# Kernel tuning notes

Measured on AMD Instinct MI355X. Metric: run time of the kernel, lower is better.

Reference implementation:

```python
import jax, jax.numpy as jnp
from jax import lax
import numpy as np

B, T, F = 4, 16000, 512          # batch, frames, enc_num_feats
NB = 24                          # 3 stacks x 8 layers
DILS = [2 ** l for _ in range(3) for l in range(8)]


def _prelu(x, a):
    return jnp.where(x >= 0, x, a * x)


def _conv(x, w, stride=1, pad=0, dil=1, groups=1):
    # x: [B,C,T], w: [O, C//groups, K]
    return lax.conv_general_dilated(x, w, (stride,), [(pad, pad)], rhs_dilation=(dil,),
                                    dimension_numbers=('NCH', 'OIH', 'NCH'),
                                    feature_group_count=groups)


def _tconv(x, w, stride=1):
    # torch ConvTranspose1d, weight layout [in, out, k], padding=0
    k = w.shape[-1]
    wf = jnp.flip(w, -1).transpose(1, 0, 2)  # [out, in, k]
    return lax.conv_general_dilated(x, wf, (1,), [(k - 1, k - 1)], lhs_dilation=(stride,),
                                    dimension_numbers=('NCH', 'OIH', 'NCH'))


def _pw(x, w, b):
    # 1x1 conv as GEMM; w: [O,C], b: [O]
    return jnp.einsum('oc,bct->bot', w, x) + b[:, None]


def _branch(x, p):
    # encoder
    f = _conv(x, p['enc_w0'], stride=8)                       # [B,512,1999]
    f = _prelu(_conv(f, p['enc_w1']), p['enc_a'][0])          # [B,512,1997]
    f = _prelu(_conv(f, p['enc_w2']), p['enc_a'][1])          # [B,512,1995]
    # mask generator (TCN)
    o = _pw(f, p['mg_in_w'], p['mg_in_b'])                    # [B,128,t]
    for i in range(NB):
        d = DILS[i]
        h = _prelu(_pw(o, p['blk_w1'][i], p['blk_b1'][i]), p['blk_a1'][i])     # [B,32,t]
        h = _conv(h, p['blk_dw'][i][:, None, :], pad=d, dil=d, groups=32) + p['blk_db'][i][:, None]
        h = _prelu(h, p['blk_a2'][i])
        if i < NB - 1:  # last block has no residual path
            o = o + _pw(h, p['blk_rw'][i], p['blk_rb'][i])
        o = o + _pw(h, p['blk_sw'][i], p['blk_sb'][i])
    m = jax.nn.sigmoid(_pw(_prelu(o, p['mg_out_a']), p['mg_out_w'], p['mg_out_b']))  # [B,1024,t]
    b, _, t = f.shape
    m = m.reshape(b, 2, F, t)
    y = (m * f[:, None]).reshape(b * 2, F, t)
    # decoder
    y = _prelu(_tconv(y, p['dec_w1']), p['dec_a'][0])
    y = _prelu(_tconv(y, p['dec_w2']), p['dec_a'][1])
    y = _tconv(y, p['dec_w3'], stride=8)                      # [2B,1,T]
    return y.reshape(b, 2, -1)


_NAMES = ['x_real', 'x_imag', 'enc_w0', 'enc_w1', 'enc_w2', 'enc_a', 'mg_in_w', 'mg_in_b',
          'blk_w1', 'blk_b1', 'blk_a1', 'blk_dw', 'blk_db', 'blk_a2', 'blk_rw', 'blk_rb',
          'blk_sw', 'blk_sb', 'mg_out_a', 'mg_out_w', 'mg_out_b', 'dec_w1', 'dec_w2', 'dec_a', 'dec_w3']


def _forward(*args):
    p = dict(zip(_NAMES, args))
    out_r = _branch(p['x_real'], p)
    out_i = _branch(p['x_imag'], p)
    return jnp.stack([out_r, out_i])  # [2, B, 2, T]; axis0 = (real, imag)


def setup_inputs() -> dict:
    key = jax.random.key(0)
    ks = jax.random.split(key, 16)
    n = lambda k, s, sc: jax.random.normal(k, s, dtype=jnp.float32) * sc
    f32 = jnp.float32
    return {
        'x_real': jax.random.normal(ks[0], (B, 1, T), dtype=f32),
        'x_imag': jax.random.normal(ks[1], (B, 1, T), dtype=f32),
        'enc_w0': n(ks[2], (512, 1, 16), 0.1),
        'enc_w1': n(ks[3], (512, 512, 3), 0.03),
        'enc_w2': n(ks[4], (512, 512, 3), 0.03),
        'enc_a': jnp.full((2,), 0.25, f32),
        'mg_in_w': n(ks[5], (128, 512), 0.05),
        'mg_in_b': jnp.zeros((128,), f32),
        'blk_w1': n(ks[6], (NB, 32, 128), 0.08),
        'blk_b1': jnp.zeros((NB, 32), f32),
        'blk_a1': jnp.full((NB,), 0.25, f32),
        'blk_dw': n(ks[7], (NB, 32, 3), 0.2),
        'blk_db': jnp.zeros((NB, 32), f32),
        'blk_a2': jnp.full((NB,), 0.25, f32),
        'blk_rw': n(ks[8], (NB, 128, 32), 0.08),  # index NB-1 unused (no_residual)
        'blk_rb': jnp.zeros((NB, 128), f32),
        'blk_sw': n(ks[9], (NB, 128, 32), 0.08),
        'blk_sb': jnp.zeros((NB, 128), f32),
        'mg_out_a': jnp.asarray(0.25, f32),
        'mg_out_w': n(ks[10], (1024, 128), 0.08),
        'mg_out_b': jnp.zeros((1024,), f32),
        'dec_w1': n(ks[11], (512, 512, 3), 0.03),
        'dec_w2': n(ks[12], (512, 512, 3), 0.03),
        'dec_a': jnp.full((2,), 0.25, f32),
        'dec_w3': n(ks[13], (512, 1, 16), 0.1),
    }


def reference(x_real, x_imag, enc_w0, enc_w1, enc_w2, enc_a, mg_in_w, mg_in_b,
              blk_w1, blk_b1, blk_a1, blk_dw, blk_db, blk_a2, blk_rw, blk_rb,
              blk_sw, blk_sb, mg_out_a, mg_out_w, mg_out_b, dec_w1, dec_w2, dec_a, dec_w3):
    return _forward(x_real, x_imag, enc_w0, enc_w1, enc_w2, enc_a, mg_in_w, mg_in_b,
                    blk_w1, blk_b1, blk_a1, blk_dw, blk_db, blk_a2, blk_rw, blk_rb,
                    blk_sw, blk_sb, mg_out_a, mg_out_w, mg_out_b, dec_w1, dec_w2, dec_a, dec_w3)
```

## Files before the change

kernel.cpp:

```cpp
#include <hip/hip_runtime.h>
#include <hip/hip_cooperative_groups.h>

namespace cg = cooperative_groups;


typedef unsigned short u16;
typedef __attribute__((ext_vector_type(8))) short bf16x8_t;
typedef __attribute__((ext_vector_type(4))) float f32x4_t;

#define ST    2064
#define HALO  8
#define TR    2064
#define RHALO 8

#define U_F0H   0ULL
#define U_F1H   8454144ULL
#define F_F2    8454144ULL
#define F_D2    0ULL
#define U_YH    33816576ULL
#define U_D1H   50724864ULL
#define F_O     33816576ULL
#define F_G0    35930112ULL
#define F_G1    36458496ULL
#define F_W     36986880ULL
#define W_MGIN  0ULL
#define W_MGOUT 65536ULL
#define W_W1T   196608ULL
#define W_WSUMT 294912ULL
#define W_BSUM  393216ULL
#define U_WB    74766336ULL
#define F_FLAG  38956032ULL
#define F_G2    38964224ULL
#define F_G3    39492608ULL
#define U_MGB   73973760ULL
#define U_MKB   74104832ULL
#define U_W1B   74375168ULL
#define U_WSB   74563584ULL

#define WS_HI 0
#define WS_LO 5120
#define W1_HI 10240
#define W1_LO 14592
#define OB_HI 0
#define OB_LO 8704
#define HB_HI 0
#define HB_LO 2560

__device__ __forceinline__ float prelu_f(float x, float a) { return x >= 0.f ? x : a * x; }
__device__ __forceinline__ u16 f2b(float f) {
    unsigned u = __float_as_uint(f);
    return (u16)((u + 0x7FFF + ((u >> 16) & 1)) >> 16);
}
__device__ __forceinline__ float b2f(u16 h) {
    return __uint_as_float((unsigned)h << 16);
}
__device__ __forceinline__ void gload16(const void* g, void* l) {
    __builtin_amdgcn_global_load_lds(
        (const __attribute__((address_space(1))) unsigned*)g,
        (__attribute__((address_space(3))) unsigned*)l, 16, 0, 0);
}

__global__ __launch_bounds__(256) void prep_all(
    const float* __restrict__ ew1, const float* __restrict__ ew2,
    const float* __restrict__ dw1, const float* __restrict__ dw2,
    const float* __restrict__ mgin_w, const float* __restrict__ mgout_w,
    const float* __restrict__ bw1, const float* __restrict__ brw,
    const float* __restrict__ brb, const float* __restrict__ bsw,
    const float* __restrict__ bsb, float* __restrict__ wsf, u16* __restrict__ wsb,
    unsigned* __restrict__ flags)
{
    const int task = blockIdx.y;
    const int idx  = blockIdx.x * 256 + threadIdx.x;
    const int stride = gridDim.x * 256;
    if (task < 4) {
        const float* src = (task == 0) ? ew1 : (task == 1) ? ew2 : (task == 2) ? dw1 : dw2;
        u16* dst = wsb + U_WB + (size_t)task * 786432ULL;
        const bool dec = (task >= 2);
        for (int n = idx; n < 786432; n += stride) {
            int j = n >> 18, o = (n >> 9) & 511, c = n & 511;
            float v = dec ? src[(size_t)c * 1536 + o * 3 + (2 - j)]
                          : src[(size_t)o * 1536 + c * 3 + j];
            dst[n] = f2b(v);
        }
    } else if (task == 4) {
        u16* dst = wsb + U_MGB;
        for (int n = idx; n < 131072; n += stride) {
            int C = n & 511, m = (n >> 9) & 127, p = n >> 16;
            float v = mgin_w[(size_t)m * 512 + C];
            u16 hh = f2b(v);
            if (p) hh = f2b(v - b2f(hh));
            dst[n] = hh;
        }
    } else if (task == 5) {
        u16* dst = wsb + U_MKB;
        for (int n = idx; n < 262144; n += stride) {
            int C = n & 127, m = (n >> 7) & 1023, p = n >> 17;
            float v = mgout_w[(size_t)m * 128 + C];
            u16 hh = f2b(v);
            if (p) hh = f2b(v - b2f(hh));
            dst[n] = hh;
        }
    } else if (task == 6) {
        float* dstf = wsf + F_W + W_W1T;
        for (int n = idx; n < 4096; n += stride) {
            int cc = n & 31, C = n >> 5;
            dstf[n] = bw1[(size_t)cc * 128 + C];
        }
        u16* dstb = wsb + U_W1B;
        for (int n = idx; n < 188416; n += stride) {
            int C = n & 127, cgi = (n >> 7) & 31, p = (n >> 12) & 1, ii = n >> 13;
            float v = bw1[(size_t)(ii + 1) * 4096 + cgi * 128 + C];
            u16 hh = f2b(v);
            if (p) hh = f2b(v - b2f(hh));
            dstb[n] = hh;
        }
    } else if (task == 7) {
        u16* dst = wsb + U_WSB;
        for (int n = idx; n < 196608; n += stride) {
            int cc = n & 31, C = (n >> 5) & 127, p = (n >> 12) & 1, i = n >> 13;
            float v = bsw[(size_t)i * 4096 + C * 32 + cc];
            if (i < 23) v += brw[(size_t)i * 4096 + C * 32 + cc];
            u16 hh = f2b(v);
            if (p) hh = f2b(v - b2f(hh));
            dst[n] = hh;
        }
    } else if (task == 8) {
        float* dst = wsf + F_W + W_BSUM;
        for (int n = idx; n < 3072; n += stride) {
            int i = n >> 7;
            float v = bsb[n];
            if (i < 23) v += brb[n];
            dst[n] = v;
        }
    } else if (task == 9) {
        const unsigned long long uoff[4] = { U_F0H, U_F1H, U_YH, U_D1H };
        const int nbArr[4]   = { 8, 8, 16, 16 };
        const int trArr[4]   = { 1999, 1997, 1995, 1997 };
#pragma unroll
        for (int z = 0; z < 4; z++) {
            unsigned* base = (unsigned*)(wsb + uoff[z]);
            const int nb = nbArr[z], Treal = trArr[z];
            const int prcnt = TR - Treal;
            const int total = nb * prcnt * 256;
            for (int n = idx; n < total; n += stride) {
                const int col = n & 255;
                const int r   = n >> 8;
                const int bb  = r / prcnt;
                const int pr  = r % prcnt;
                const int row = (pr < RHALO) ? pr : (Treal + pr);
                base[((size_t)bb * TR + row) * 256 + col] = 0u;
            }
        }
    } else {
        for (int n = idx; n < 4096; n += stride) flags[n] = 0u;
    }
}

__global__ __launch_bounds__(256) void enc0_kernel(
    const float* __restrict__ xr, const float* __restrict__ xi,
    const float* __restrict__ w0, u16* __restrict__ f0h)
{
    const int t  = blockIdx.x * 256 + threadIdx.x;
    const int c0 = blockIdx.y * 8;
    const int b  = blockIdx.z;
    if (t >= 1999) return;
    const float* x = (b < 4) ? (xr + (size_t)b * 16000) : (xi + (size_t)(b - 4) * 16000);
    float xv[16];
    const int base = t * 8;
#pragma unroll
    for (int k = 0; k < 16; k++) xv[k] = x[base + k];
    union { u16 u[8]; uint4 v; } p;
#pragma unroll
    for (int cq = 0; cq < 8; cq++) {
        const float* w = w0 + (size_t)(c0 + cq) * 16;
        float acc = 0.f;
#pragma unroll
        for (int k = 0; k < 16; k++) acc = fmaf(xv[k], w[k], acc);
        p.u[cq] = f2b(acc);
    }
    *(uint4*)&f0h[((size_t)b * TR + RHALO + t) * 512 + c0] = p.v;
}

template <int JOFF, int OUTF32, int TT>
__global__ __launch_bounds__(256) void conv_mfma(
    const u16* __restrict__ in, u16* __restrict__ out16, float* __restrict__ out32,
    const u16* __restrict__ wM, const float* __restrict__ alpha_p, int Tout)
{
    constexpr int NF    = TT / 32;
    constexpr int BFULL = TT / 64;
    constexpr int SMEMSZ = (TT == 128) ? 17408 : 14464;
    __shared__ __align__(16) u16 smem[SMEMSZ];
    u16* As = smem;
    u16* Bs = smem + 12288;
    const int tid  = threadIdx.x;
    const int t0   = blockIdx.x * TT;
    const int ob   = blockIdx.y * 128;
    const int b    = blockIdx.z;
    const int l15  = tid & 15;
    const int quad = (tid >> 4) & 3;
    const int wave = tid >> 6;
    const int wm   = (wave & 1) * 64;
    const int wn   = (wave >> 1) * (TT / 2);
    const u16* inb = in + (size_t)b * TR * 512;
    const int wvb  = wave * 1024;

    f32x4_t acc[4][NF];
#pragma unroll
    for (int i = 0; i < 4; i++)
#pragma unroll
        for (int k = 0; k < NF; k++) acc[i][k] = (f32x4_t){0.f, 0.f, 0.f, 0.f};

    for (int c0 = 0; c0 < 512; c0 += 32) {
#pragma unroll
        for (int k = 0; k < 6; k++) {
            const int v = k * 256 + tid;
            const int j = v >> 9, r = (v >> 2) & 127, c = v & 3;
            const int cg = c ^ ((r >> 1) & 3);
            gload16(&wM[((size_t)(j * 512 + ob + r)) * 512 + c0 + cg * 8],
                    (char*)As + k * 4096 + wvb);
        }
#pragma unroll
        for (int k = 0; k < BFULL; k++) {
            const int v = k * 256 + tid;
            const int r = v >> 2, c = v & 3;
            const int cg = c ^ ((r >> 1) & 3);
            gload16(&inb[(size_t)(RHALO + t0 + JOFF + r) * 512 + c0 + cg * 8],
                    (char*)Bs + k * 4096 + wvb);
        }
        if (tid < 16) {
            const int v = BFULL * 256 + tid;
            const int r = v >> 2, c = v & 3;
            const int cg = c ^ ((r >> 1) & 3);
            gload16(&inb[(size_t)(RHALO + t0 + JOFF + r) * 512 + c0 + cg * 8],
                    (char*)Bs + BFULL * 4096);
        }
        __syncthreads();
#pragma unroll
        for (int j = 0; j < 3; j++) {
            bf16x8_t aw[4], bi[NF];
#pragma unroll
            for (int mf = 0; mf < 4; mf++) {
                const int row = wm + mf * 16 + l15;
                const int ch  = quad ^ ((row >> 1) & 3);
                aw[mf] = *(const bf16x8_t*)&As[j * 4096 + row * 32 + ch * 8];
            }
#pragma unroll
            for (int nf = 0; nf < NF; nf++) {
                const int row = wn + nf * 16 + l15 + j;
                const int ch  = quad ^ ((row >> 1) & 3);
                bi[nf] = *(const bf16x8_t*)&Bs[row * 32 + ch * 8];
            }
#pragma unroll
            for (int mf = 0; mf < 4; mf++)
#pragma unroll
                for (int nf = 0; nf < NF; nf++) {
                    if (OUTF32)
                        acc[mf][nf] = __builtin_amdgcn_mfma_f32_16x16x32_bf16(
                            bi[nf], aw[mf], acc[mf][nf], 0, 0, 0);
                    else
                        acc[mf][nf] = __builtin_amdgcn_mfma_f32_16x16x32_bf16(
                            aw[mf], bi[nf], acc[mf][nf], 0, 0, 0);
                }
        }
        __syncthreads();
    }

    const float alpha = *alpha_p;
    if (!OUTF32) {
        u16* tile = smem;
#pragma unroll
        for (int mf = 0; mf < 4; mf++)
#pragma unroll
            for (int nf = 0; nf < NF; nf++) {
                const int t_loc = wn + nf * 16 + l15;
                const int c_loc = wm + mf * 16 + quad * 4;
                f32x4_t a = acc[mf][nf];
                ushort4 s;
                s.x = f2b(prelu_f(a.x, alpha));
                s.y = f2b(prelu_f(a.y, alpha));
                s.z = f2b(prelu_f(a.z, alpha));
                s.w = f2b(prelu_f(a.w, alpha));
                *(ushort4*)&tile[t_loc * 136 + c_loc] = s;
            }
        __syncthreads();
        for (int v = tid; v < TT * 16; v += 256) {
            const int row = v >> 4, seg = v & 15;
            const int t = t0 + row;
            if (t < Tout)
                *(uint4*)&out16[((size_t)b * TR + RHALO + t) * 512 + ob + seg * 8] =
                    *(const uint4*)&tile[row * 136 + seg * 8];
        }
    } else {
#pragma unroll
        for (int mf = 0; mf < 4; mf++)
#pragma unroll
            for (int nf = 0; nf < NF; nf++) {
                const int o  = ob + wm + mf * 16 + l15;
                const int tb = t0 + wn + nf * 16 + quad * 4;
                f32x4_t a = acc[mf][nf];
                float v0 = prelu_f(a.x, alpha), v1 = prelu_f(a.y, alpha);
                float v2 = prelu_f(a.z, alpha), v3 = prelu_f(a.w, alpha);
                float* p = out32 + ((size_t)(b * 512 + o)) * ST + HALO + tb;
                if (tb + 3 < Tout) {
                    *(float4*)p = make_float4(v0, v1, v2, v3);
                } else {
                    if (tb + 0 < Tout) p[0] = v0;
                    if (tb + 1 < Tout) p[1] = v1;
                    if (tb + 2 < Tout) p[2] = v2;
                    if (tb + 3 < Tout) p[3] = v3;
                }
            }
    }
}

__global__ __launch_bounds__(256) void mgin_kernel(
    const float* __restrict__ f2, float* __restrict__ o_buf, float* __restrict__ g_out,
    const u16* __restrict__ wA, const float* __restrict__ bias,
    const float* __restrict__ w1T0, const float* __restrict__ b1_0,
    const float* __restrict__ a1_0)
{
    __shared__ __align__(16) u16   As[8192];
    __shared__ __align__(16) u16   Bsm[5120];
    __shared__ __align__(16) float o_lds[128 * 68];
    const int tid = threadIdx.x;
    const int t0  = blockIdx.x * 64;
    const int b   = blockIdx.y;
    const int l15 = tid & 15, quad = (tid >> 4) & 3, wave = tid >> 6;
    const int wm  = wave * 32;
    const int bc  = tid >> 3;
    const int bs  = tid & 7;

    f32x4_t acc[2][4];
#pragma unroll
    for (int mf = 0; mf < 2; mf++)
#pragma unroll
        for (int nf = 0; nf < 4; nf++) acc[mf][nf] = (f32x4_t){0.f, 0.f, 0.f, 0.f};

    for (int ks = 0; ks < 16; ks++) {
#pragma unroll
        for (int k = 0; k < 4; k++) {
            const int v = k * 256 + tid;
            const int p = v >> 9, r = (v >> 2) & 127, c = v & 3;
            const int cg = c ^ ((r >> 1) & 3);
            gload16(&wA[(size_t)p * 65536 + (size_t)r * 512 + ks * 32 + cg * 8],
                    (char*)As + k * 4096 + wave * 1024);
        }
        {
            const float* src = f2 + (size_t)(b * 512 + ks * 32 + bc) * ST + HALO + t0 + bs * 8;
            float4 v0 = *(const float4*)src;
            float4 v1 = *(const float4*)(src + 4);
            const float vv[8] = {v0.x, v0.y, v0.z, v0.w, v1.x, v1.y, v1.z, v1.w};
#pragma unroll
            for (int j = 0; j < 8; j++) {
                const int t = bs * 8 + j;
                const u16 hh = f2b(vv[j]);
                Bsm[t * 40 + bc] = hh;
                Bsm[2560 + t * 40 + bc] = f2b(vv[j] - b2f(hh));
            }
        }
        __syncthreads();
        bf16x8_t ah[2], al[2], bh[4], bl[4];
#pragma unroll
        for (int mf = 0; mf < 2; mf++) {
            const int row = wm + mf * 16 + l15;
            const int ch  = quad ^ ((row >> 1) & 3);
            ah[mf] = *(const bf16x8_t*)&As[row * 32 + ch * 8];
            al[mf] = *(const bf16x8_t*)&As[4096 + row * 32 + ch * 8];
        }
#pragma unroll
        for (int nf = 0; nf < 4; nf++) {
            const int rt = nf * 16 + l15;
            bh[nf] = *(const bf16x8_t*)&Bsm[rt * 40 + quad * 8];
            bl[nf] = *(const bf16x8_t*)&Bsm[2560 + rt * 40 + quad * 8];
        }
#pragma unroll
        for (int mf = 0; mf < 2; mf++)
#pragma unroll
            for (int nf = 0; nf < 4; nf++) {
                acc[mf][nf] = __builtin_amdgcn_mfma_f32_16x16x32_bf16(al[mf], bh[nf], acc[mf][nf], 0, 0, 0);
                acc[mf][nf] = __builtin_amdgcn_mfma_f32_16x16x32_bf16(ah[mf], bl[nf], acc[mf][nf], 0, 0, 0);
                acc[mf][nf] = __builtin_amdgcn_mfma_f32_16x16x32_bf16(ah[mf], bh[nf], acc[mf][nf], 0, 0, 0);
            }
        __syncthreads();
    }

#pragma unroll
    for (int mf = 0; mf < 2; mf++)
#pragma unroll
        for (int nf = 0; nf < 4; nf++) {
#pragma unroll
            for (int r = 0; r < 4; r++) {
                const int m = wm + mf * 16 + quad * 4 + r;
                o_lds[m * 68 + nf * 16 + l15] = acc[mf][nf][r] + bias[m];
            }
        }
    __syncthreads();

    for (int n = tid; n < 2048; n += 256) {
        const int row = n >> 4, seg = n & 15;
        const int tb = t0 + seg * 4;
        float* dst = o_buf + (size_t)(b * 128 + row) * ST + HALO + tb;
        const float* srcl = &o_lds[row * 68 + seg * 4];
        if (tb + 3 < 1995) {
            *(float4*)dst = *(const float4*)srcl;
        } else {
#pragma unroll
            for (int kk = 0; kk < 4; kk++)
                if (tb + kk < 1995) dst[kk] = srcl[kk];
        }
    }

    const int t = tid & 63, cg_ = tid >> 6;
    const float a1 = *a1_0;
    float acc2[8];
#pragma unroll
    for (int q = 0; q < 8; q++) acc2[q] = b1_0[cg_ * 8 + q];
    for (int C = 0; C < 128; C++) {
        const float ov = o_lds[C * 68 + t];
        const float4* wr = (const float4*)(w1T0 + (size_t)C * 32 + cg_ * 8);
        float4 w0 = wr[0], w1 = wr[1];
        acc2[0] = fmaf(w0.x, ov, acc2[0]); acc2[1] = fmaf(w0.y, ov, acc2[1]);
        acc2[2] = fmaf(w0.z, ov, acc2[2]); acc2[3] = fmaf(w0.w, ov, acc2[3]);
        acc2[4] = fmaf(w1.x, ov, acc2[4]); acc2[5] = fmaf(w1.y, ov, acc2[5]);
        acc2[6] = fmaf(w1.z, ov, acc2[6]); acc2[7] = fmaf(w1.w, ov, acc2[7]);
    }
    const int tt = t0 + t;
    if (tt < 1995) {
#pragma unroll
        for (int q = 0; q < 8; q++)
            g_out[(size_t)(b * 32 + cg_ * 8 + q) * ST + HALO + tt] = prelu_f(acc2[q], a1);
    }
}

__device__ __forceinline__ void poll_acquire(const unsigned* flags, int b, int j,
                                             int k, unsigned target)
{
    int lo = j - k; if (lo < 0) lo = 0;
    int hi = j + k; if (hi > 31) hi = 31;
    for (int n = lo; n <= hi; n++) {
        if (n == j) continue;
        const unsigned* p = flags + ((b << 5) + n) * 16;
        while (__hip_atomic_load(p, __ATOMIC_RELAXED, __HIP_MEMORY_SCOPE_AGENT) < target)
            __builtin_amdgcn_s_sleep(2);
    }
    __builtin_amdgcn_fence(__ATOMIC_ACQUIRE, "agent");
}

__device__ __forceinline__ void store_pair_agent(float* dst, int trel, float v0, float v1)
{
    if (trel + 1 < 1995) {
        unsigned long long raw =
            ((unsigned long long)__float_as_uint(v1) << 32) | __float_as_uint(v0);
        __hip_atomic_store((unsigned long long*)dst, raw,
                           __ATOMIC_RELAXED, __HIP_MEMORY_SCOPE_AGENT);
    } else if (trel < 1995) {
        __hip_atomic_store(dst, v0, __ATOMIC_RELAXED, __HIP_MEMORY_SCOPE_AGENT);
    }
}

__global__ __launch_bounds__(512) void tcn_fused(
    float* __restrict__ g0, float* __restrict__ g1,
    float* __restrict__ g2, float* __restrict__ g3,
    float* __restrict__ o_buf,
    const float* __restrict__ dw_all, const float* __restrict__ db_all,
    const float* __restrict__ a2_all,
    const u16* __restrict__ wsb16, const float* __restrict__ bsum_all,
    const u16* __restrict__ w1b16, const float* __restrict__ b1_all,
    const float* __restrict__ a1_all, unsigned* __restrict__ wflag)
{
    __shared__ __align__(16) u16  wbuf[18944];
    __shared__ __align__(16) u16  hbuf[5120];
    __shared__ __align__(16) u16  ob16[17408];
    __shared__ __align__(16) float g_lds[2][2176];
    __shared__ __align__(16) float halo_lds[8320];

    const int tid = threadIdx.x;
    const int blk = blockIdx.x;
    const int b   = blk & 7;
    const int jt  = blk >> 3;
    const int t0  = jt * 64;
    float* gbuf[4] = { g0, g1, g2, g3 };

    const int wv   = tid >> 6;
    const int l15  = tid & 15;
    const int quad = (tid >> 4) & 3;
    const int Cb   = wv * 16 + quad * 4;

    f32x4_t o_acc[4];
#pragma unroll
    for (int k = 0; k < 4; k++)
#pragma unroll
        for (int r = 0; r < 4; r++)
            o_acc[k][r] = o_buf[((size_t)(b * 128 + Cb + r)) * ST + HALO + t0 + k * 16 + l15];
    {
        int cc = tid >> 4, seg = tid & 15;
        *(float4*)&g_lds[0][cc * 68 + seg * 4] =
            *(const float4*)&g0[((size_t)(b * 32 + cc)) * ST + HALO + t0 + seg * 4];
    }

    for (int i = 0; i < 24; i++) {
        const int dil  = 1 << (i & 7);
        const int dil2 = (dil < 2) ? 2 : dil;
        const int k_rd = (dil > 64) ? 2 : 1;
        const float* gin_g = gbuf[i & 3];
        float* gout_g      = gbuf[(i + 1) & 3];
        float* gin_lds  = g_lds[i & 1];
        float* gout_lds = g_lds[(i + 1) & 1];

        {
            const u16* wsg = wsb16 + (size_t)i * 8192;
#pragma unroll
            for (int k = 0; k < 2; k++) {
                int c = tid + k * 512;
                int p = c >> 9, r = (c >> 2) & 127, s = c & 3;
                *(uint4*)&wbuf[(p ? WS_LO : WS_HI) + r * 40 + s * 8] =
                    *(const uint4*)&wsg[c * 8];
            }
            if (i < 23) {
                const u16* w1g = w1b16 + (size_t)i * 8192;
#pragma unroll
                for (int k = 0; k < 2; k++) {
                    int c = tid + k * 512;
                    int p = c >> 9, cgi = (c >> 4) & 31, s = c & 15;
                    *(uint4*)&wbuf[(p ? W1_LO : W1_HI) + cgi * 136 + s * 8] =
                        *(const uint4*)&w1g[c * 8];
                }
            }
        }

        if (i > 0 && tid == 0) poll_acquire(wflag, b, jt, k_rd, (unsigned)i);
        __syncthreads();

        {
            const int dsh = (dil2 >= 128) ? 7 : (dil2 >= 64) ? 6 : (dil2 >= 32) ? 5
                          : (dil2 >= 16) ? 4 : (dil2 >= 8) ? 3 : (dil2 >= 4) ? 2 : 1;
            const int total = 32 << dsh;
            for (int n = tid; n < total; n += 512) {
                const int cc = n >> dsh;
                const int pi = n & (dil2 - 1);
                const int hc = pi * 2;
                const int tg = (hc < dil2) ? (t0 - dil2 + hc) : (t0 + 64 + hc - dil2);
                float v0 = 0.f, v1 = 0.f;
                const float* src = gin_g + ((size_t)(b * 32 + cc)) * ST + HALO + tg;
                if (tg >= 0 && tg + 1 < 1995) {
                    unsigned long long raw = __hip_atomic_load(
                        (const unsigned long long*)src,
                        __ATOMIC_RELAXED, __HIP_MEMORY_SCOPE_AGENT);
                    v0 = __uint_as_float((unsigned)raw);
                    v1 = __uint_as_float((unsigned)(raw >> 32));
                } else {
                    if (tg >= 0 && tg < 1995)
                        v0 = __hip_atomic_load(src, __ATOMIC_RELAXED,
                                               __HIP_MEMORY_SCOPE_AGENT);
                    if (tg + 1 >= 0 && tg + 1 < 1995)
                        v1 = __hip_atomic_load(src + 1, __ATOMIC_RELAXED,
                                               __HIP_MEMORY_SCOPE_AGENT);
                }
                halo_lds[cc * 260 + hc]     = v0;
                halo_lds[cc * 260 + hc + 1] = v1;
            }
        }
        __syncthreads();

        {
            const float a2 = a2_all[i];
            const int t = tid & 63, cc0 = (tid >> 6) * 4;
            const int tt = t0 + t;
            ushort4 hi4, lo4;
            u16 hs[4], ls[4];
#pragma unroll
            for (int q = 0; q < 4; q++) {
                const int cc = cc0 + q;
                const float w0 = dw_all[i * 96 + cc * 3 + 0];
                const float w1v = dw_all[i * 96 + cc * 3 + 1];
                const float w2 = dw_all[i * 96 + cc * 3 + 2];
                const float ctr = gin_lds[cc * 68 + t];
                float lo = 0.f, hi = 0.f;
                const int tm = tt - dil;
                if (tm >= 0)
                    lo = (tm >= t0) ? gin_lds[cc * 68 + (tm - t0)]
                                    : halo_lds[cc * 260 + (tm - t0 + dil2)];
                const int tp = tt + dil;
                if (tp < 1995)
                    hi = (tp < t0 + 64) ? gin_lds[cc * 68 + (tp - t0)]
                                        : halo_lds[cc * 260 + (dil2 + tp - t0 - 64)];
                float s = db_all[i * 32 + cc] + w1v * ctr;
                s = fmaf(w0, lo, s);
                s = fmaf(w2, hi, s);
                const float hval = prelu_f(s, a2);
                const u16 hh = f2b(hval);
                hs[q] = hh;
                ls[q] = f2b(hval - b2f(hh));
            }
            hi4.x = hs[0]; hi4.y = hs[1]; hi4.z = hs[2]; hi4.w = hs[3];
            lo4.x = ls[0]; lo4.y = ls[1]; lo4.z = ls[2]; lo4.w = ls[3];
            *(ushort4*)&hbuf[HB_HI + t * 40 + cc0] = hi4;
            *(ushort4*)&hbuf[HB_LO + t * 40 + cc0] = lo4;
        }
        __syncthreads();

        {
            const bf16x8_t a_hi = *(const bf16x8_t*)&wbuf[WS_HI + (wv * 16 + l15) * 40 + quad * 8];
            const bf16x8_t a_lo = *(const bf16x8_t*)&wbuf[WS_LO + (wv * 16 + l15) * 40 + quad * 8];
            const float4 bs4 = *(const float4*)&bsum_all[i * 128 + Cb];
#pragma unroll
            for (int k = 0; k < 4; k++) {
                const bf16x8_t b_hi = *(const bf16x8_t*)&hbuf[HB_HI + (k * 16 + l15) * 40 + quad * 8];
                const bf16x8_t b_lo = *(const bf16x8_t*)&hbuf[HB_LO + (k * 16 + l15) * 40 + quad * 8];
                f32x4_t acc = o_acc[k];
                acc = __builtin_amdgcn_mfma_f32_16x16x32_bf16(a_lo, b_hi, acc, 0, 0, 0);
                acc = __builtin_amdgcn_mfma_f32_16x16x32_bf16(a_hi, b_lo, acc, 0, 0, 0);
                acc = __builtin_amdgcn_mfma_f32_16x16x32_bf16(a_hi, b_hi, acc, 0, 0, 0);
                acc.x += bs4.x; acc.y += bs4.y; acc.z += bs4.z; acc.w += bs4.w;
                o_acc[k] = acc;
            }
        }

        if (i == 23) break;

#pragma unroll
        for (int k = 0; k < 4; k++) {
            ushort4 hi4, lo4;
            u16 hs[4], ls[4];
#pragma unroll
            for (int r = 0; r < 4; r++) {
                const float v = o_acc[k][r];
                const u16 hh = f2b(v);
                hs[r] = hh;
                ls[r] = f2b(v - b2f(hh));
            }
            hi4.x = hs[0]; hi4.y = hs[1]; hi4.z = hs[2]; hi4.w = hs[3];
            lo4.x = ls[0]; lo4.y = ls[1]; lo4.z = ls[2]; lo4.w = ls[3];
            const int t_loc = k * 16 + l15;
            *(ushort4*)&ob16[OB_HI + t_loc * 136 + Cb] = hi4;
            *(ushort4*)&ob16[OB_LO + t_loc * 136 + Cb] = lo4;
        }
        __syncthreads();

        {
            const int cgb = (wv & 1) * 16;
            const int tb  = (wv >> 1) * 16;
            const float4 b14 = *(const float4*)&b1_all[(i + 1) * 32 + cgb + quad * 4];
            f32x4_t ga = (f32x4_t){b14.x, b14.y, b14.z, b14.w};
            f32x4_t gc = (f32x4_t){0.f, 0.f, 0.f, 0.f};
#pragma unroll
            for (int slab = 0; slab < 4; slab++) {
                const bf16x8_t wa_hi = *(const bf16x8_t*)&wbuf[W1_HI + (cgb + l15) * 136 + slab * 32 + quad * 8];
                const bf16x8_t wa_lo = *(const bf16x8_t*)&wbuf[W1_LO + (cgb + l15) * 136 + slab * 32 + quad * 8];
                const bf16x8_t obh   = *(const bf16x8_t*)&ob16[OB_HI + (tb + l15) * 136 + slab * 32 + quad * 8];
                const bf16x8_t obl   = *(const bf16x8_t*)&ob16[OB_LO + (tb + l15) * 136 + slab * 32 + quad * 8];
                if (slab & 1) {
                    gc = __builtin_amdgcn_mfma_f32_16x16x32_bf16(wa_lo, obh, gc, 0, 0, 0);
                    gc = __builtin_amdgcn_mfma_f32_16x16x32_bf16(wa_hi, obl, gc, 0, 0, 0);
                    gc = __builtin_amdgcn_mfma_f32_16x16x32_bf16(wa_hi, obh, gc, 0, 0, 0);
                } else {
                    ga = __builtin_amdgcn_mfma_f32_16x16x32_bf16(wa_lo, obh, ga, 0, 0, 0);
                    ga = __builtin_amdgcn_mfma_f32_16x16x32_bf16(wa_hi, obl, ga, 0, 0, 0);
                    ga = __builtin_amdgcn_mfma_f32_16x16x32_bf16(wa_hi, obh, ga, 0, 0, 0);
                }
            }
            const float a1 = a1_all[i + 1];
#pragma unroll
            for (int r = 0; r < 4; r++) {
                const int cgr = cgb + quad * 4 + r;
                gout_lds[cgr * 68 + tb + l15] = prelu_f(ga[r] + gc[r], a1);
            }
        }
        __syncthreads();

        {
            const int dnext = 1 << ((i + 1) & 7);
            int md2 = (dnext > 64) ? 64 : dnext;
            if (md2 < 2) md2 = 2;
            if (md2 >= 64) {
                for (int n = tid; n < 1024; n += 512) {
                    const int cc = n >> 5, pi = n & 31;
                    const int lt = pi * 2;
                    float* dst = gout_g + ((size_t)(b * 32 + cc)) * ST + HALO + t0 + lt;
                    store_pair_agent(dst, t0 + lt,
                                     gout_lds[cc * 68 + lt], gout_lds[cc * 68 + lt + 1]);
                }
            } else {
                const int msh = (md2 >= 32) ? 5 : (md2 >= 16) ? 4 : (md2 >= 8) ? 3
                              : (md2 >= 4) ? 2 : 1;
                const int total = 32 << msh;
                for (int n = tid; n < total; n += 512) {
                    const int cc = n >> msh;
                    const int pi = n & (md2 - 1);
                    const int hc = pi * 2;
                    const int lt = (hc < md2) ? hc : (64 - 2 * md2 + hc);
                    float* dst = gout_g + ((size_t)(b * 32 + cc)) * ST + HALO + t0 + lt;
                    store_pair_agent(dst, t0 + lt,
                                     gout_lds[cc * 68 + lt], gout_lds[cc * 68 + lt + 1]);
                }
            }
        }
        __syncthreads();

        if (tid == 0)
            __hip_atomic_store(&wflag[((b << 5) + jt) * 16], (unsigned)(i + 1),
                               __ATOMIC_RELAXED, __HIP_MEMORY_SCOPE_AGENT);
    }

#pragma unroll
    for (int k = 0; k < 4; k++)
#pragma unroll
        for (int r = 0; r < 4; r++)
            o_buf[((size_t)(b * 128 + Cb + r)) * ST + HALO + t0 + k * 16 + l15] = o_acc[k][r];
}

__global__ __launch_bounds__(256) void mask_kernel(
    const float* __restrict__ o_buf, const float* __restrict__ f2, u16* __restrict__ yh,
    const u16* __restrict__ wA, const float* __restrict__ mb,
    const float* __restrict__ a_out_p)
{
    __shared__ __align__(16) u16 smem[33792];
    u16* As = smem;
    u16* ob = smem + 16384;

    const int tid  = threadIdx.x;
    const int t0   = blockIdx.x * 64;
    const int m0   = blockIdx.y * 256;
    const int b    = blockIdx.z;
    const float ao = *a_out_p;
    const int l15  = tid & 15;
    const int quad = (tid >> 4) & 3;
    const int wave = tid >> 6;
    const int wm   = wave * 64;

    {
        const int C = tid >> 1, th = (tid & 1) * 32;
        const float* orow = o_buf + (size_t)(b * 128 + C) * ST + HALO + t0 + th;
#pragma unroll
        for (int q = 0; q < 8; q++) {
            float4 v = *(const float4*)(orow + q * 4);
            const float vv[4] = {v.x, v.y, v.z, v.w};
#pragma unroll
            for (int j = 0; j < 4; j++) {
                const float pv = prelu_f(vv[j], ao);
                const u16 hh = f2b(pv);
                const int t = th + q * 4 + j;
                ob[OB_HI + t * 136 + C] = hh;
                ob[OB_LO + t * 136 + C] = f2b(pv - b2f(hh));
            }
        }
    }

    f32x4_t acc[4][4];
#pragma unroll
    for (int mf = 0; mf < 4; mf++)
#pragma unroll
        for (int nf = 0; nf < 4; nf++) acc[mf][nf] = (f32x4_t){0.f, 0.f, 0.f, 0.f};

    for (int ks = 0; ks < 4; ks++) {
#pragma unroll
        for (int k = 0; k < 8; k++) {
            const int v = k * 256 + tid;
            const int p = v >> 10, r = (v >> 2) & 255, c = v & 3;
            const int cg = c ^ ((r >> 1) & 3);
            gload16(&wA[(size_t)p * 131072 + (size_t)(m0 + r) * 128 + ks * 32 + cg * 8],
                    (char*)As + k * 4096 + wave * 1024);
        }
        __syncthreads();
        bf16x8_t ah[4], al[4], bh[4], bl[4];
#pragma unroll
        for (int mf = 0; mf < 4; mf++) {
            const int row = wm + mf * 16 + l15;
            const int ch  = quad ^ ((row >> 1) & 3);
            ah[mf] = *(const bf16x8_t*)&As[row * 32 + ch * 8];
            al[mf] = *(const bf16x8_t*)&As[8192 + row * 32 + ch * 8];
        }
#pragma unroll
        for (int nf = 0; nf < 4; nf++) {
            const int rt = nf * 16 + l15;
            bh[nf] = *(const bf16x8_t*)&ob[OB_HI + rt * 136 + ks * 32 + quad * 8];
            bl[nf] = *(const bf16x8_t*)&ob[OB_LO + rt * 136 + ks * 32 + quad * 8];
        }
#pragma unroll
        for (int mf = 0; mf < 4; mf++)
#pragma unroll
            for (int nf = 0; nf < 4; nf++) {
                acc[mf][nf] = __builtin_amdgcn_mfma_f32_16x16x32_bf16(al[mf], bh[nf], acc[mf][nf], 0, 0, 0);
                acc[mf][nf] = __builtin_amdgcn_mfma_f32_16x16x32_bf16(ah[mf], bl[nf], acc[mf][nf], 0, 0, 0);
                acc[mf][nf] = __builtin_amdgcn_mfma_f32_16x16x32_bf16(ah[mf], bh[nf], acc[mf][nf], 0, 0, 0);
            }
        __syncthreads();
    }

    const int F0 = m0 & 511, sIdx = m0 >> 9;
    u16* tile = smem;
#pragma unroll
    for (int mf = 0; mf < 4; mf++)
#pragma unroll
        for (int nf = 0; nf < 4; nf++) {
            const int tl = nf * 16 + l15;
            u16 sv[4];
#pragma unroll
            for (int r = 0; r < 4; r++) {
                const int mloc = wm + mf * 16 + quad * 4 + r;
                const float x = acc[mf][nf][r] + mb[m0 + mloc];
                const float mval = 1.f / (1.f + __expf(-x));
                const float y = mval *
                    f2[(size_t)(b * 512 + F0 + mloc) * ST + HALO + t0 + tl];
                sv[r] = f2b(y);
            }
            ushort4 s;
            s.x = sv[0]; s.y = sv[1]; s.z = sv[2]; s.w = sv[3];
            *(ushort4*)&tile[tl * 264 + wm + mf * 16 + quad * 4] = s;
        }
    __syncthreads();
    u16* ybase = yh + ((size_t)(b * 2 + sIdx) * TR) * 512;
    for (int v = tid; v < 2048; v += 256) {
        const int row = v >> 5, seg = v & 31;
        const int t = t0 + row;
        if (t < 1995)
            *(uint4*)&ybase[(size_t)(RHALO + t) * 512 + F0 + seg * 8] =
                *(const uint4*)&tile[row * 264 + seg * 8];
    }
}

__global__ __launch_bounds__(256) void dec3_kernel(
    const float* __restrict__ d2, const float* __restrict__ w3, float* __restrict__ out)
{
    __shared__ float tile[512][34];
    const int tid = threadIdx.x;
    const int bb  = blockIdx.y;
    const int tau0 = blockIdx.x * 256;
    const int tbase = (tau0 >> 3) - 1;
    const float* src = d2 + (size_t)bb * 512 * ST + HALO + tbase;
    for (int n = tid; n < 512 * 34; n += 256) {
        int o = n / 34, i = n % 34;
        const int tg = tbase + i;
        tile[o][i] = (tg >= 0 && tg < 1999) ? src[(size_t)o * ST + i] : 0.f;
    }
    __syncthreads();

    const int tau = tau0 + tid;
    if (tau >= 16000) return;
    const int k1 = tau & 7;
    const int t1l = (tid >> 3) + 1;
    float acc = 0.f;
#pragma unroll 8
    for (int o = 0; o < 512; o++) {
        acc = fmaf(tile[o][t1l],     w3[o * 16 + k1],     acc);
        acc = fmaf(tile[o][t1l - 1], w3[o * 16 + 8 + k1], acc);
    }
    const int p = bb >> 1, s = bb & 1;
    out[(size_t)(p * 2 + s) * 16000 + tau] = acc;
}

extern "C" void kernel_launch(void* const* d_in, const int* in_sizes, int n_in,
                              void* d_out, int out_size, void* d_ws, size_t ws_size,
                              hipStream_t stream)
{
    (void)in_sizes; (void)n_in; (void)out_size; (void)ws_size;
    float* ws  = (float*)d_ws;
    u16*   wsu = (u16*)d_ws;
    const float* x_real   = (const float*)d_in[0];
    const float* x_imag   = (const float*)d_in[1];
    const float* enc_w0   = (const float*)d_in[2];
    const float* enc_w1   = (const float*)d_in[3];
    const float* enc_w2   = (const float*)d_in[4];
    const float* enc_a    = (const float*)d_in[5];
    const float* mg_in_w  = (const float*)d_in[6];
    const float* mg_in_b  = (const float*)d_in[7];
    const float* blk_w1   = (const float*)d_in[8];
    const float* blk_b1   = (const float*)d_in[9];
    const float* blk_a1   = (const float*)d_in[10];
    const float* blk_dw   = (const float*)d_in[11];
    const float* blk_db   = (const float*)d_in[12];
    const float* blk_a2   = (const float*)d_in[13];
    const float* blk_rw   = (const float*)d_in[14];
    const float* blk_rb   = (const float*)d_in[15];
    const float* blk_sw   = (const float*)d_in[16];
    const float* blk_sb   = (const float*)d_in[17];
    const float* mg_out_a = (const float*)d_in[18];
    const float* mg_out_w = (const float*)d_in[19];
    const float* mg_out_b = (const float*)d_in[20];
    const float* dec_w1   = (const float*)d_in[21];
    const float* dec_w2   = (const float*)d_in[22];
    const float* dec_a    = (const float*)d_in[23];
    const float* dec_w3   = (const float*)d_in[24];
    float* out = (float*)d_out;

    u16*   f0h   = wsu + U_F0H;
    u16*   f1h   = wsu + U_F1H;
    float* f2    = ws  + F_F2;
    float* d2    = ws  + F_D2;
    u16*   yh    = wsu + U_YH;
    u16*   d1h   = wsu + U_D1H;
    float* obuf  = ws  + F_O;
    float* g0    = ws  + F_G0;
    float* g1    = ws  + F_G1;
    float* g2    = ws  + F_G2;
    float* g3    = ws  + F_G3;
    float* WF    = ws  + F_W;
    u16*   WB    = wsu + U_WB;
    unsigned* flags = (unsigned*)(ws + F_FLAG);

    const dim3 blk(256);

    prep_all<<<dim3(64, 11), blk, 0, stream>>>(enc_w1, enc_w2, dec_w1, dec_w2,
        mg_in_w, mg_out_w, blk_w1, blk_rw, blk_rb, blk_sw, blk_sb, ws, wsu, flags);

    enc0_kernel<<<dim3(8, 64, 8), blk, 0, stream>>>(x_real, x_imag, enc_w0, f0h);

    conv_mfma<0, 0, 64><<<dim3(32, 4, 8), blk, 0, stream>>>(
        f0h, f1h, nullptr, WB + 0 * 786432, enc_a + 0, 1997);
    conv_mfma<0, 1, 64><<<dim3(32, 4, 8), blk, 0, stream>>>(
        f1h, nullptr, f2, WB + 1 * 786432, enc_a + 1, 1995);

    mgin_kernel<<<dim3(32, 8), blk, 0, stream>>>(f2, obuf, g0, wsu + U_MGB, mg_in_b,
        WF + W_W1T, blk_b1, blk_a1);

    {
        const float* dwp   = blk_dw;
        const float* dbp   = blk_db;
        const float* a2p   = blk_a2;
        const u16*   wsbp  = wsu + U_WSB;
        const float* bsump = WF + W_BSUM;
        const u16*   w1bp  = wsu + U_W1B;
        const float* b1p   = blk_b1;
        const float* a1p   = blk_a1;
        unsigned* flg = flags;
        void* args[] = { &g0, &g1, &g2, &g3, &obuf,
                         (void*)&dwp, (void*)&dbp, (void*)&a2p,
                         (void*)&wsbp, (void*)&bsump, (void*)&w1bp,
                         (void*)&b1p, (void*)&a1p, &flg };
        (void)hipLaunchCooperativeKernel((void*)tcn_fused, dim3(256), dim3(512),
                                         args, 0, stream);
    }

    mask_kernel<<<dim3(32, 4, 8), blk, 0, stream>>>(obuf, f2, yh,
        wsu + U_MKB, mg_out_b, mg_out_a);

    conv_mfma<-2, 0, 128><<<dim3(16, 4, 16), blk, 0, stream>>>(
        yh, d1h, nullptr, WB + 2 * 786432, dec_a + 0, 1997);
    conv_mfma<-2, 1, 128><<<dim3(16, 4, 16), blk, 0, stream>>>(
        d1h, nullptr, d2, WB + 3 * 786432, dec_a + 1, 1999);

    dec3_kernel<<<dim3(63, 16), blk, 0, stream>>>(d2, dec_w3, out);
}
```

Baseline: 708.7 us.

## Double-buffer conv_mfma LDS stages and restructure dec3 channel reduction

The MFMA conv kernel now stages one tap's weight slice and each 32-channel input slice into ping-pong LDS buffers, prefetching the next stage while computing the current one, so global loads overlap with MFMA work instead of being serialized behind a barrier. The output-tile scratch size is recomputed to fit the larger buffer layout. Separately, the dec3 transposed-conv kernel now has each thread compute all 8 output phases over a strided subset of channels using vectorized weight loads, then combine them with a cross-lane shuffle reduction, with the LDS tile padded to stride 35 to avoid bank conflicts. The pipeline adds a barrier per tap step (48 per tile instead of 32) and raises LDS use, which may lower occupancy.

```diff
diff --git a/kernel.cpp b/kernel.cpp
--- a/kernel.cpp
+++ b/kernel.cpp
@@ -187,11 +187,13 @@
     const u16* __restrict__ wM, const float* __restrict__ alpha_p, int Tout)
 {
     constexpr int NF    = TT / 32;
-    constexpr int BFULL = TT / 64;
-    constexpr int SMEMSZ = (TT == 128) ? 17408 : 14464;
+    constexpr int BROWS = TT + 4;
+    constexpr int BSZ   = BROWS * 32;
+    constexpr int BUFSZ = 8192 + 2 * BSZ;
+    constexpr int TILESZ = TT * 136;
+    constexpr int SMEMSZ = (BUFSZ > TILESZ) ? BUFSZ : TILESZ;
     __shared__ __align__(16) u16 smem[SMEMSZ];
-    u16* As = smem;
-    u16* Bs = smem + 12288;
+
     const int tid  = threadIdx.x;
     const int t0   = blockIdx.x * TT;
     const int ob   = blockIdx.y * 128;
@@ -210,58 +212,75 @@
 #pragma unroll
         for (int k = 0; k < NF; k++) acc[i][k] = (f32x4_t){0.f, 0.f, 0.f, 0.f};
 
-    for (int c0 = 0; c0 < 512; c0 += 32) {
-#pragma unroll
-        for (int k = 0; k < 6; k++) {
-            const int v = k * 256 + tid;
-            const int j = v >> 9, r = (v >> 2) & 127, c = v & 3;
+    auto stageA = [&](int k1) {
+        const int j = k1 % 3, c0 = (k1 / 3) * 32;
+        char* dst = (char*)smem + ((k1 & 1) << 13);
+#pragma unroll
+        for (int kk = 0; kk < 2; kk++) {
+            const int v = kk * 256 + tid;
+            const int r = v >> 2, c = v & 3;
             const int cg = c ^ ((r >> 1) & 3);
             gload16(&wM[((size_t)(j * 512 + ob + r)) * 512 + c0 + cg * 8],
-                    (char*)As + k * 4096 + wvb);
-        }
-#pragma unroll
-        for (int k = 0; k < BFULL; k++) {
-            const int v = k * 256 + tid;
+                    dst + kk * 4096 + wvb);
+        }
+    };
+    auto stageB = [&](int ci) {
+        const int c0 = ci * 32;
+        char* dst = (char*)(smem + 8192 + (ci & 1) * BSZ);
+#pragma unroll
+        for (int kk = 0; kk < TT / 64; kk++) {
+            const int v = kk * 256 + tid;
             const int r = v >> 2, c = v & 3;
             const int cg = c ^ ((r >> 1) & 3);
             gload16(&inb[(size_t)(RHALO + t0 + JOFF + r) * 512 + c0 + cg * 8],
-                    (char*)Bs + k * 4096 + wvb);
+                    dst + kk * 4096 + wvb);
         }
         if (tid < 16) {
-            const int v = BFULL * 256 + tid;
+            const int v = (TT / 64) * 256 + tid;
             const int r = v >> 2, c = v & 3;
             const int cg = c ^ ((r >> 1) & 3);
             gload16(&inb[(size_t)(RHALO + t0 + JOFF + r) * 512 + c0 + cg * 8],
-                    (char*)Bs + BFULL * 4096);
-        }
-        __syncthreads();
-#pragma unroll
-        for (int j = 0; j < 3; j++) {
-            bf16x8_t aw[4], bi[NF];
-#pragma unroll
-            for (int mf = 0; mf < 4; mf++) {
-                const int row = wm + mf * 16 + l15;
-                const int ch  = quad ^ ((row >> 1) & 3);
-                aw[mf] = *(const bf16x8_t*)&As[j * 4096 + row * 32 + ch * 8];
-            }
+                    dst + (TT / 64) * 4096);
+        }
+    };
+
+    stageA(0);
+    stageB(0);
+    __syncthreads();
+
+#pragma unroll 6
+    for (int k = 0; k < 48; k++) {
+        if (k < 47) {
+            stageA(k + 1);
+            if ((k + 1) % 3 == 0) stageB((k + 1) / 3);
+        }
+        const int j = k % 3;
+        const u16* Ac = smem + ((k & 1) << 12);
+        const u16* Bc = smem + 8192 + ((k / 3) & 1) * BSZ;
+        bf16x8_t aw[4], bi[NF];
+#pragma unroll
+        for (int mf = 0; mf < 4; mf++) {
+            const int row = wm + mf * 16 + l15;
+            const int ch  = quad ^ ((row >> 1) & 3);
+            aw[mf] = *(const bf16x8_t*)&Ac[row * 32 + ch * 8];
+        }
+#pragma unroll
+        for (int nf = 0; nf < NF; nf++) {
+            const int row = wn + nf * 16 + l15 + j;
+            const int ch  = quad ^ ((row >> 1) & 3);
+            bi[nf] = *(const bf16x8_t*)&Bc[row * 32 + ch * 8];
+        }
+#pragma unroll
+        for (int mf = 0; mf < 4; mf++)
 #pragma unroll
             for (int nf = 0; nf < NF; nf++) {
-                const int row = wn + nf * 16 + l15 + j;
-                const int ch  = quad ^ ((row >> 1) & 3);
-                bi[nf] = *(const bf16x8_t*)&Bs[row * 32 + ch * 8];
-            }
-#pragma unroll
-            for (int mf = 0; mf < 4; mf++)
-#pragma unroll
-                for (int nf = 0; nf < NF; nf++) {
-                    if (OUTF32)
-                        acc[mf][nf] = __builtin_amdgcn_mfma_f32_16x16x32_bf16(
-                            bi[nf], aw[mf], acc[mf][nf], 0, 0, 0);
-                    else
-                        acc[mf][nf] = __builtin_amdgcn_mfma_f32_16x16x32_bf16(
-                            aw[mf], bi[nf], acc[mf][nf], 0, 0, 0);
-                }
-        }
+                if (OUTF32)
+                    acc[mf][nf] = __builtin_amdgcn_mfma_f32_16x16x32_bf16(
+                        bi[nf], aw[mf], acc[mf][nf], 0, 0, 0);
+                else
+                    acc[mf][nf] = __builtin_amdgcn_mfma_f32_16x16x32_bf16(
+                        aw[mf], bi[nf], acc[mf][nf], 0, 0, 0);
+            }
         __syncthreads();
     }
 
@@ -822,7 +841,7 @@
 __global__ __launch_bounds__(256) void dec3_kernel(
     const float* __restrict__ d2, const float* __restrict__ w3, float* __restrict__ out)
 {
-    __shared__ float tile[512][34];
+    __shared__ float tile[512 * 35];
     const int tid = threadIdx.x;
     const int bb  = blockIdx.y;
     const int tau0 = blockIdx.x * 256;
@@ -831,22 +850,47 @@
     for (int n = tid; n < 512 * 34; n += 256) {
         int o = n / 34, i = n % 34;
         const int tg = tbase + i;
-        tile[o][i] = (tg >= 0 && tg < 1999) ? src[(size_t)o * ST + i] : 0.f;
+        tile[o * 35 + i] = (tg >= 0 && tg < 1999) ? src[(size_t)o * ST + i] : 0.f;
     }
     __syncthreads();
 
-    const int tau = tau0 + tid;
-    if (tau >= 16000) return;
-    const int k1 = tau & 7;
-    const int t1l = (tid >> 3) + 1;
-    float acc = 0.f;
-#pragma unroll 8
-    for (int o = 0; o < 512; o++) {
-        acc = fmaf(tile[o][t1l],     w3[o * 16 + k1],     acc);
-        acc = fmaf(tile[o][t1l - 1], w3[o * 16 + 8 + k1], acc);
-    }
-    const int p = bb >> 1, s = bb & 1;
-    out[(size_t)(p * 2 + s) * 16000 + tau] = acc;
+    const int oc = tid & 7;
+    const int tl = tid >> 3;
+    float acc[8];
+#pragma unroll
+    for (int q = 0; q < 8; q++) acc[q] = 0.f;
+#pragma unroll 4
+    for (int m = 0; m < 64; m++) {
+        const int o = oc + m * 8;
+        const float v1 = tile[o * 35 + tl + 1];
+        const float v0 = tile[o * 35 + tl];
+        const float4 wa = *(const float4*)&w3[o * 16 + 0];
+        const float4 wb = *(const float4*)&w3[o * 16 + 4];
+        const float4 wc = *(const float4*)&w3[o * 16 + 8];
+        const float4 wd = *(const float4*)&w3[o * 16 + 12];
+        acc[0] = fmaf(v1, wa.x, fmaf(v0, wc.x, acc[0]));
+        acc[1] = fmaf(v1, wa.y, fmaf(v0, wc.y, acc[1]));
+        acc[2] = fmaf(v1, wa.z, fmaf(v0, wc.z, acc[2]));
+        acc[3] = fmaf(v1, wa.w, fmaf(v0, wc.w, acc[3]));
+        acc[4] = fmaf(v1, wb.x, fmaf(v0, wd.x, acc[4]));
+        acc[5] = fmaf(v1, wb.y, fmaf(v0, wd.y, acc[5]));
+        acc[6] = fmaf(v1, wb.z, fmaf(v0, wd.z, acc[6]));
+        acc[7] = fmaf(v1, wb.w, fmaf(v0, wd.w, acc[7]));
+    }
+#pragma unroll
+    for (int s = 1; s < 8; s <<= 1)
+#pragma unroll
+        for (int q = 0; q < 8; q++)
+            acc[q] += __shfl_xor(acc[q], s, 64);
+    float r = acc[0];
+#pragma unroll
+    for (int q = 1; q < 8; q++) if (oc == q) r = acc[q];
+
+    const int tau = tau0 + tl * 8 + oc;
+    if (tau < 16000) {
+        const int p = bb >> 1, s = bb & 1;
+        out[(size_t)(p * 2 + s) * 16000 + tau] = r;
+    }
 }
 
 extern "C" void kernel_launch(void* const* d_in, const int* in_sizes, int n_in,
```

Measured after the change: 738.4 us. +4.2%, slower.
